# Kernel optimization log

Measured on AMD Instinct MI355X. Metric: run time of the kernel, lower is better.

The kernel has to match this reference:

```python
import jax, jax.numpy as jnp
import numpy as np

D_MODEL = 512
NUM_HEADS = 8
D_HEAD = D_MODEL // NUM_HEADS


def setup_inputs() -> dict:
    key = jax.random.key(0)
    kx, kq, kk, kv, ko = jax.random.split(key, 5)
    s = 1.0 / np.sqrt(D_MODEL)
    return {
        "X": jax.random.normal(kx, (2, 4096, D_MODEL), dtype=jnp.float32),
        "Wq": jax.random.normal(kq, (D_MODEL, D_MODEL), dtype=jnp.float32) * s,
        "Wk": jax.random.normal(kk, (D_MODEL, D_MODEL), dtype=jnp.float32) * s,
        "Wv": jax.random.normal(kv, (D_MODEL, D_MODEL), dtype=jnp.float32) * s,
        "Wo": jax.random.normal(ko, (D_MODEL, D_MODEL), dtype=jnp.float32) * s,
    }


def reference(X, Wq, Wk, Wv, Wo):
    B, L, D = X.shape
    H, dh = NUM_HEADS, D_HEAD
    # Linear projections (torch Linear: y = x @ W.T), split heads -> [B, H, L, dh]
    def proj(W):
        return (X @ W.T).reshape(B, L, H, dh).transpose(0, 2, 1, 3)
    Q, K, V = proj(Wq), proj(Wk), proj(Wv)
    # Scaled dot-product attention; scores [B, H, L, L]
    scores = jnp.einsum("bhqd,bhkd->bhqk", Q, K) / jnp.sqrt(jnp.asarray(dh, X.dtype))
    attn = jax.nn.softmax(scores, axis=-1)
    out = jnp.einsum("bhqk,bhkd->bhqd", attn, V)  # [B, H, L, dh]
    out = out.transpose(0, 2, 1, 3).reshape(B, L, D)
    return out @ Wo.T
```

## Files before the change

### kernel.cpp

```cpp
#include <hip/hip_runtime.h>
#include <math.h>

#define D_MODEL 512
#define NHEADS  8
#define DH      64
#define LSEQ    4096
#define NB      2
#define M_TOT   (NB * LSEQ)
#define NSPLIT  2
#define KHALF   (LSEQ / NSPLIT)

typedef __attribute__((ext_vector_type(8))) short bf16x8;
typedef __attribute__((ext_vector_type(4))) float f32x4;
typedef __attribute__((ext_vector_type(8))) unsigned short ushort8v;

#define MFMA16(a, b, c) __builtin_amdgcn_mfma_f32_16x16x32_bf16(a, b, c, 0, 0, 0)

__device__ __forceinline__ ushort f2bf(float x) {
    unsigned u = __builtin_bit_cast(unsigned, x);
    u += 0x7fffu + ((u >> 16) & 1u);
    return (ushort)(u >> 16);
}

__device__ __forceinline__ float bf2f(ushort u) {
    unsigned v = ((unsigned)u) << 16;
    return __builtin_bit_cast(float, v);
}

__device__ __forceinline__ unsigned cvt_pk_bf16(float a, float b) {
    unsigned r;
    asm("v_cvt_pk_bf16_f32 %0, %1, %2" : "=v"(r) : "v"(a), "v"(b));
    return r;
}

__device__ __forceinline__ float fexp2(float x) {
#if __has_builtin(__builtin_amdgcn_exp2f)
    return __builtin_amdgcn_exp2f(x);
#else
    return exp2f(x);
#endif
}

__device__ __forceinline__ void gload16(const void* g, void* l) {
    __builtin_amdgcn_global_load_lds(
        (const __attribute__((address_space(1))) unsigned*)g,
        (__attribute__((address_space(3))) unsigned*)l, 16, 0, 0);
}

__global__ __launch_bounds__(256) void cast_all(
    const float* __restrict__ X,  const float* __restrict__ Wq,
    const float* __restrict__ Wk, const float* __restrict__ Wv,
    const float* __restrict__ Wo,
    ushort* __restrict__ Xb,  ushort* __restrict__ Wqb,
    ushort* __restrict__ Wkb, ushort* __restrict__ Wvb,
    ushort* __restrict__ Wob)
{
    const int seg = blockIdx.y;
    const float* src = seg == 0 ? X : seg == 1 ? Wq : seg == 2 ? Wk
                      : seg == 3 ? Wv : Wo;
    ushort* dst = seg == 0 ? Xb : seg == 1 ? Wqb : seg == 2 ? Wkb
                 : seg == 3 ? Wvb : Wob;
    const int n = (seg == 0) ? M_TOT * D_MODEL : D_MODEL * D_MODEL;
    const int idx = (blockIdx.x * 256 + threadIdx.x) * 8;
    if (idx >= n) return;
    float4 a = *(const float4*)(src + idx);
    float4 b = *(const float4*)(src + idx + 4);
    ushort8v o;
    o[0] = f2bf(a.x); o[1] = f2bf(a.y); o[2] = f2bf(a.z); o[3] = f2bf(a.w);
    o[4] = f2bf(b.x); o[5] = f2bf(b.y); o[6] = f2bf(b.z); o[7] = f2bf(b.w);
    *(ushort8v*)(dst + idx) = o;
}

__device__ __forceinline__ void gemm_core(
    const ushort* __restrict__ A, const ushort* __restrict__ Bw,
    ushort (*Alds)[64], ushort (*Blds)[64], f32x4 acc[4][4],
    int m0, int n0, int w, int lg, int lr)
{
    const int tid = threadIdx.x;
    const int wr = w >> 1, wc = w & 1;
    const int srow = tid >> 3;
    const int scol = (tid & 7) * 8;

    for (int k0 = 0; k0 < D_MODEL; k0 += 64) {
        __syncthreads();
        #pragma unroll
        for (int i = 0; i < 4; ++i) {
            gload16(A  + (size_t)(m0 + i * 32 + srow) * D_MODEL + k0 + scol,
                    (char*)Alds + i * 4096 + w * 1024);
            gload16(Bw + (size_t)(n0 + i * 32 + srow) * D_MODEL + k0 + scol,
                    (char*)Blds + i * 4096 + w * 1024);
        }
        __syncthreads();
        #pragma unroll
        for (int kk = 0; kk < 2; ++kk) {
            bf16x8 af[4], bfr[4];
            #pragma unroll
            for (int i = 0; i < 4; ++i)
                af[i] = *(const bf16x8*)&Alds[wr * 64 + 16 * i + lr][kk * 32 + 8 * lg];
            #pragma unroll
            for (int j = 0; j < 4; ++j)
                bfr[j] = *(const bf16x8*)&Blds[wc * 64 + 16 * j + lr][kk * 32 + 8 * lg];
            #pragma unroll
            for (int i = 0; i < 4; ++i)
                #pragma unroll
                for (int j = 0; j < 4; ++j)
                    acc[i][j] = MFMA16(af[i], bfr[j], acc[i][j]);
        }
    }
}

__global__ __launch_bounds__(256) void gemm_qkv(
    const ushort* __restrict__ Xb,
    const ushort* __restrict__ Wqb, const ushort* __restrict__ Wkb,
    const ushort* __restrict__ Wvb,
    ushort* __restrict__ Qb, ushort* __restrict__ Kb, ushort* __restrict__ Vtb)
{
    __shared__ __align__(16) ushort Alds[128][64];
    __shared__ __align__(16) ushort Blds[128][64];

    const int mode = blockIdx.z;
    const ushort* Bw = mode == 0 ? Wqb : mode == 1 ? Wkb : Wvb;

    const int tid = threadIdx.x;
    const int w = tid >> 6, l = tid & 63;
    const int lg = l >> 4, lr = l & 15;
    const int wr = w >> 1, wc = w & 1;
    const int m0 = blockIdx.x * 128;
    const int n0 = blockIdx.y * 128;

    f32x4 acc[4][4];
    #pragma unroll
    for (int i = 0; i < 4; ++i)
        #pragma unroll
        for (int j = 0; j < 4; ++j) acc[i][j] = (f32x4){0.f, 0.f, 0.f, 0.f};

    gemm_core(Xb, Bw, Alds, Blds, acc, m0, n0, w, lg, lr);

    if (mode < 2) {
        const float scale = (mode == 0) ? 0.125f * 1.44269504088896f : 1.0f;
        ushort* Yb = (mode == 0) ? Qb : Kb;
        #pragma unroll
        for (int i = 0; i < 4; ++i) {
            const int mb = m0 + wr * 64 + 16 * i + 4 * lg;
            const int b = mb >> 12, lq = mb & 4095;
            #pragma unroll
            for (int j = 0; j < 4; ++j) {
                const int ng = n0 + wc * 64 + 16 * j + lr;
                const int h = ng >> 6, dh = ng & 63;
                ushort* Yp = Yb + ((size_t)(b * NHEADS + h) * LSEQ + lq) * DH + dh;
                #pragma unroll
                for (int r = 0; r < 4; ++r)
                    Yp[(size_t)r * DH] = f2bf(acc[i][j][r] * scale);
            }
        }
    } else {
        #pragma unroll
        for (int i = 0; i < 4; ++i) {
            const int mb = m0 + wr * 64 + 16 * i + 4 * lg;
            const int b = mb >> 12, lq = mb & 4095;
            #pragma unroll
            for (int j = 0; j < 4; ++j) {
                const int ng = n0 + wc * 64 + 16 * j + lr;
                const int h = ng >> 6, dh = ng & 63;
                ushort4 w4;
                w4.x = f2bf(acc[i][j][0]); w4.y = f2bf(acc[i][j][1]);
                w4.z = f2bf(acc[i][j][2]); w4.w = f2bf(acc[i][j][3]);
                *(ushort4*)(Vtb + ((size_t)(b * NHEADS + h) * DH + dh) * LSEQ + lq) = w4;
            }
        }
    }
}

__global__ __launch_bounds__(256) void gemm_wo(
    const ushort* __restrict__ Cb, const ushort* __restrict__ Wob,
    float* __restrict__ out)
{
    __shared__ __align__(16) ushort Alds[128][64];
    __shared__ __align__(16) ushort Blds[128][64];

    const int tid = threadIdx.x;
    const int w = tid >> 6, l = tid & 63;
    const int lg = l >> 4, lr = l & 15;
    const int wr = w >> 1, wc = w & 1;
    const int m0 = blockIdx.x * 128;
    const int n0 = blockIdx.y * 128;

    f32x4 acc[4][4];
    #pragma unroll
    for (int i = 0; i < 4; ++i)
        #pragma unroll
        for (int j = 0; j < 4; ++j) acc[i][j] = (f32x4){0.f, 0.f, 0.f, 0.f};

    gemm_core(Cb, Wob, Alds, Blds, acc, m0, n0, w, lg, lr);

    #pragma unroll
    for (int i = 0; i < 4; ++i) {
        const int mb = m0 + wr * 64 + 16 * i + 4 * lg;
        #pragma unroll
        for (int j = 0; j < 4; ++j) {
            const int ng = n0 + wc * 64 + 16 * j + lr;
            float* Yp = out + (size_t)mb * D_MODEL + ng;
            #pragma unroll
            for (int r = 0; r < 4; ++r)
                Yp[(size_t)r * D_MODEL] = acc[i][j][r];
        }
    }
}

#define QBLK 128
#define KBLK 64

__global__ __launch_bounds__(256) void flash_mfma(
    const ushort* __restrict__ Q, const ushort* __restrict__ K,
    const ushort* __restrict__ Vt, ushort* __restrict__ Op,
    float* __restrict__ Ls)
{
    __shared__ __align__(16) ushort Klds[64][68];
    __shared__ __align__(16) ushort Vlds[64][68];
    __shared__ __align__(16) ushort Plds[128][68];

    const int tid = threadIdx.x;
    const int w  = tid >> 6;
    const int l  = tid & 63;
    const int lg = l >> 4;
    const int lr = l & 15;

    const int bh = blockIdx.y;
    const int q0 = blockIdx.x * QBLK;
    const int z  = blockIdx.z;
    const int kt0  = z * KHALF;
    const int kend = kt0 + KHALF;

    bf16x8 qa[2][2];
    #pragma unroll
    for (int u = 0; u < 2; ++u) {
        const ushort* qp = Q + ((size_t)bh * LSEQ + q0 + 32 * w + 16 * u + lr) * DH + 8 * lg;
        qa[u][0] = *(const bf16x8*)(qp);
        qa[u][1] = *(const bf16x8*)(qp + 32);
    }

    float lsum[2] = {0.f, 0.f};
    f32x4 o4[2][4];
    #pragma unroll
    for (int u = 0; u < 2; ++u)
        #pragma unroll
        for (int ot = 0; ot < 4; ++ot) o4[u][ot] = (f32x4){0.f, 0.f, 0.f, 0.f};

    const int srow = tid >> 2;
    const int scol = (tid & 3) << 4;
    const ushort* Kp = K  + (size_t)bh * LSEQ * DH;
    const ushort* Vp = Vt + (size_t)bh * DH * LSEQ;

    uint4 kA, kB, vA, vB;
    {
        const ushort* ks = Kp + (size_t)(kt0 + srow) * DH + scol;
        const ushort* vs = Vp + (size_t)srow * LSEQ + kt0 + scol;
        kA = *(const uint4*)(ks); kB = *(const uint4*)(ks + 8);
        vA = *(const uint4*)(vs); vB = *(const uint4*)(vs + 8);
    }

    for (int kt = kt0; kt < kend; kt += KBLK) {
        __syncthreads();
        *(uint4*)&Klds[srow][scol] = kA;  *(uint4*)&Klds[srow][scol + 8] = kB;
        *(uint4*)&Vlds[srow][scol] = vA;  *(uint4*)&Vlds[srow][scol + 8] = vB;
        __syncthreads();

        if (kt + KBLK < kend) {
            const ushort* ks = Kp + (size_t)(kt + KBLK + srow) * DH + scol;
            const ushort* vs = Vp + (size_t)srow * LSEQ + (kt + KBLK) + scol;
            kA = *(const uint4*)(ks); kB = *(const uint4*)(ks + 8);
            vA = *(const uint4*)(vs); vB = *(const uint4*)(vs + 8);
        }

        f32x4 s[2][4];
        #pragma unroll
        for (int kt2 = 0; kt2 < 4; ++kt2) {
            bf16x8 k0 = *(const bf16x8*)&Klds[kt2 * 16 + lr][8 * lg];
            bf16x8 k1 = *(const bf16x8*)&Klds[kt2 * 16 + lr][32 + 8 * lg];
            f32x4 z4 = (f32x4){0.f, 0.f, 0.f, 0.f};
            s[0][kt2] = MFMA16(k1, qa[0][1], MFMA16(k0, qa[0][0], z4));
            s[1][kt2] = MFMA16(k1, qa[1][1], MFMA16(k0, qa[1][0], z4));
        }

        #pragma unroll
        for (int u = 0; u < 2; ++u) {
            float rs = 0.f;
            #pragma unroll
            for (int kt2 = 0; kt2 < 4; ++kt2) {
                const float p0 = fexp2(s[u][kt2][0]);
                const float p1 = fexp2(s[u][kt2][1]);
                const float p2 = fexp2(s[u][kt2][2]);
                const float p3 = fexp2(s[u][kt2][3]);
                rs += (p0 + p1) + (p2 + p3);
                uint2 pw;
                pw.x = cvt_pk_bf16(p0, p1);
                pw.y = cvt_pk_bf16(p2, p3);
                *(uint2*)&Plds[32 * w + 16 * u + lr][kt2 * 16 + 4 * lg] = pw;
            }
            lsum[u] += rs;
        }

        #pragma unroll
        for (int vh = 0; vh < 2; ++vh) {
            bf16x8 p0 = *(const bf16x8*)&Plds[32 * w + lr][32 * vh + 8 * lg];
            bf16x8 p1 = *(const bf16x8*)&Plds[32 * w + 16 + lr][32 * vh + 8 * lg];
            #pragma unroll
            for (int ot = 0; ot < 4; ++ot) {
                bf16x8 vv = *(const bf16x8*)&Vlds[16 * ot + lr][32 * vh + 8 * lg];
                o4[0][ot] = MFMA16(p0, vv, o4[0][ot]);
                o4[1][ot] = MFMA16(p1, vv, o4[1][ot]);
            }
        }
    }

    const int b = bh >> 3, h = bh & 7;
    ushort* Opz = Op + (size_t)z * M_TOT * D_MODEL;
    #pragma unroll
    for (int u = 0; u < 2; ++u) {
        float t = lsum[u];
        t += __shfl_xor(t, 16);
        t += __shfl_xor(t, 32);
        if (lg == 0)
            Ls[((size_t)z * NB * NHEADS + bh) * LSEQ + q0 + 32 * w + 16 * u + lr] = t;
        #pragma unroll
        for (int r = 0; r < 4; ++r) {
            const int qrow = q0 + 32 * w + 16 * u + 4 * lg + r;
            ushort* op = Opz + ((size_t)b * LSEQ + qrow) * D_MODEL + h * DH + lr;
            #pragma unroll
            for (int ot = 0; ot < 4; ++ot)
                op[16 * ot] = f2bf(o4[u][ot][r]);
        }
    }
}

__global__ __launch_bounds__(256) void combine(
    const ushort* __restrict__ Op, const float* __restrict__ Ls,
    ushort* __restrict__ Cb)
{
    const int idx = blockIdx.x * 256 + threadIdx.x;
    const int row = idx >> 6;
    const int col0 = (idx & 63) << 3;
    const int b = row >> 12, lq = row & 4095;
    const int h = col0 >> 6;
    const int bh = b * NHEADS + h;

    const float l0 = Ls[(size_t)bh * LSEQ + lq];
    const float l1 = Ls[((size_t)NB * NHEADS + bh) * LSEQ + lq];
    const float inv = 1.0f / (l0 + l1);

    const size_t off = (size_t)row * D_MODEL + col0;
    ushort8v a0 = *(const ushort8v*)(Op + off);
    ushort8v a1 = *(const ushort8v*)(Op + (size_t)M_TOT * D_MODEL + off);
    ushort8v o;
    #pragma unroll
    for (int i = 0; i < 8; ++i)
        o[i] = f2bf((bf2f(a0[i]) + bf2f(a1[i])) * inv);
    *(ushort8v*)(Cb + off) = o;
}

extern "C" void kernel_launch(void* const* d_in, const int* in_sizes, int n_in,
                              void* d_out, int out_size, void* d_ws, size_t ws_size,
                              hipStream_t stream)
{
    const float* X  = (const float*)d_in[0];
    const float* Wq = (const float*)d_in[1];
    const float* Wk = (const float*)d_in[2];
    const float* Wv = (const float*)d_in[3];
    const float* Wo = (const float*)d_in[4];
    float* out = (float*)d_out;

    char* ws = (char*)d_ws;
    const size_t szX = (size_t)M_TOT * D_MODEL * 2;
    const size_t szW = (size_t)D_MODEL * D_MODEL * 2;
    ushort* Xb  = (ushort*)(ws);
    ushort* Wqb = (ushort*)(ws + szX);
    ushort* Wkb = (ushort*)(ws + szX + szW);
    ushort* Wvb = (ushort*)(ws + szX + 2 * szW);
    ushort* Wob = (ushort*)(ws + szX + 3 * szW);
    ushort* Qb  = (ushort*)(ws + szX + 4 * szW);
    ushort* Kb  = (ushort*)(ws + 2 * szX + 4 * szW);
    ushort* Vtb = (ushort*)(ws + 3 * szX + 4 * szW);
    ushort* Opb = (ushort*)(ws + 4 * szX + 4 * szW);
    float*  Lsb = (float*) (ws + 6 * szX + 4 * szW);
    ushort* Cbb = (ushort*)(ws + 6 * szX + 4 * szW + (size_t)NSPLIT * NB * NHEADS * LSEQ * 4);

    dim3 gc(M_TOT * D_MODEL / (256 * 8), 5);
    cast_all<<<gc, 256, 0, stream>>>(X, Wq, Wk, Wv, Wo, Xb, Wqb, Wkb, Wvb, Wob);

    dim3 gq(M_TOT / 128, D_MODEL / 128, 3);
    gemm_qkv<<<gq, 256, 0, stream>>>(Xb, Wqb, Wkb, Wvb, Qb, Kb, Vtb);

    dim3 gf(LSEQ / QBLK, NB * NHEADS, NSPLIT);
    flash_mfma<<<gf, 256, 0, stream>>>(Qb, Kb, Vtb, Opb, Lsb);

    dim3 gm(M_TOT * D_MODEL / (256 * 8));
    combine<<<gm, 256, 0, stream>>>(Opb, Lsb, Cbb);

    dim3 go(M_TOT / 128, D_MODEL / 128);
    gemm_wo<<<go, 256, 0, stream>>>(Cbb, Wob, out);
}
```

Before: 153.8 us.

## Double-buffer K/V tiles in LDS and raise MFMA wave priority

Converts the flash-attention K/V staging into a two-slot LDS ring. The next tile is written into the spare buffer while the current one is consumed, and the global prefetch runs two tiles ahead. This drops one of the two barriers per iteration. It also wraps the MFMA sections in s_setprio to favour matrix-issue waves. The cost is doubled K/V LDS use, which may reduce occupancy, plus more register-held prefetch state.

```diff
diff --git a/kernel.cpp b/kernel.cpp
--- a/kernel.cpp
+++ b/kernel.cpp
@@ -209,14 +209,15 @@
 
 #define QBLK 128
 #define KBLK 64
+#define NT   (KHALF / KBLK)
 
 __global__ __launch_bounds__(256) void flash_mfma(
     const ushort* __restrict__ Q, const ushort* __restrict__ K,
     const ushort* __restrict__ Vt, ushort* __restrict__ Op,
     float* __restrict__ Ls)
 {
-    __shared__ __align__(16) ushort Klds[64][68];
-    __shared__ __align__(16) ushort Vlds[64][68];
+    __shared__ __align__(16) ushort Klds[2][64][68];
+    __shared__ __align__(16) ushort Vlds[2][64][68];
     __shared__ __align__(16) ushort Plds[128][68];
 
     const int tid = threadIdx.x;
@@ -228,8 +229,7 @@
     const int bh = blockIdx.y;
     const int q0 = blockIdx.x * QBLK;
     const int z  = blockIdx.z;
-    const int kt0  = z * KHALF;
-    const int kend = kt0 + KHALF;
+    const int kt0 = z * KHALF;
 
     bf16x8 qa[2][2];
     #pragma unroll
@@ -257,30 +257,43 @@
         const ushort* vs = Vp + (size_t)srow * LSEQ + kt0 + scol;
         kA = *(const uint4*)(ks); kB = *(const uint4*)(ks + 8);
         vA = *(const uint4*)(vs); vB = *(const uint4*)(vs + 8);
-    }
-
-    for (int kt = kt0; kt < kend; kt += KBLK) {
-        __syncthreads();
-        *(uint4*)&Klds[srow][scol] = kA;  *(uint4*)&Klds[srow][scol + 8] = kB;
-        *(uint4*)&Vlds[srow][scol] = vA;  *(uint4*)&Vlds[srow][scol + 8] = vB;
-        __syncthreads();
-
-        if (kt + KBLK < kend) {
-            const ushort* ks = Kp + (size_t)(kt + KBLK + srow) * DH + scol;
-            const ushort* vs = Vp + (size_t)srow * LSEQ + (kt + KBLK) + scol;
+        *(uint4*)&Klds[0][srow][scol] = kA;  *(uint4*)&Klds[0][srow][scol + 8] = kB;
+        *(uint4*)&Vlds[0][srow][scol] = vA;  *(uint4*)&Vlds[0][srow][scol + 8] = vB;
+        const ushort* ks1 = Kp + (size_t)(kt0 + KBLK + srow) * DH + scol;
+        const ushort* vs1 = Vp + (size_t)srow * LSEQ + (kt0 + KBLK) + scol;
+        kA = *(const uint4*)(ks1); kB = *(const uint4*)(ks1 + 8);
+        vA = *(const uint4*)(vs1); vB = *(const uint4*)(vs1 + 8);
+    }
+    __syncthreads();
+
+    for (int t = 0; t < NT; ++t) {
+        const int cur = t & 1;
+
+        if (t + 1 < NT) {
+            *(uint4*)&Klds[cur ^ 1][srow][scol]     = kA;
+            *(uint4*)&Klds[cur ^ 1][srow][scol + 8] = kB;
+            *(uint4*)&Vlds[cur ^ 1][srow][scol]     = vA;
+            *(uint4*)&Vlds[cur ^ 1][srow][scol + 8] = vB;
+        }
+        if (t + 2 < NT) {
+            const int kt2g = kt0 + (t + 2) * KBLK;
+            const ushort* ks = Kp + (size_t)(kt2g + srow) * DH + scol;
+            const ushort* vs = Vp + (size_t)srow * LSEQ + kt2g + scol;
             kA = *(const uint4*)(ks); kB = *(const uint4*)(ks + 8);
             vA = *(const uint4*)(vs); vB = *(const uint4*)(vs + 8);
         }
 
         f32x4 s[2][4];
+        __builtin_amdgcn_s_setprio(1);
         #pragma unroll
         for (int kt2 = 0; kt2 < 4; ++kt2) {
-            bf16x8 k0 = *(const bf16x8*)&Klds[kt2 * 16 + lr][8 * lg];
-            bf16x8 k1 = *(const bf16x8*)&Klds[kt2 * 16 + lr][32 + 8 * lg];
+            bf16x8 k0 = *(const bf16x8*)&Klds[cur][kt2 * 16 + lr][8 * lg];
+            bf16x8 k1 = *(const bf16x8*)&Klds[cur][kt2 * 16 + lr][32 + 8 * lg];
             f32x4 z4 = (f32x4){0.f, 0.f, 0.f, 0.f};
             s[0][kt2] = MFMA16(k1, qa[0][1], MFMA16(k0, qa[0][0], z4));
             s[1][kt2] = MFMA16(k1, qa[1][1], MFMA16(k0, qa[1][0], z4));
         }
+        __builtin_amdgcn_s_setprio(0);
 
         #pragma unroll
         for (int u = 0; u < 2; ++u) {
@@ -300,17 +313,21 @@
             lsum[u] += rs;
         }
 
+        __builtin_amdgcn_s_setprio(1);
         #pragma unroll
         for (int vh = 0; vh < 2; ++vh) {
             bf16x8 p0 = *(const bf16x8*)&Plds[32 * w + lr][32 * vh + 8 * lg];
             bf16x8 p1 = *(const bf16x8*)&Plds[32 * w + 16 + lr][32 * vh + 8 * lg];
             #pragma unroll
             for (int ot = 0; ot < 4; ++ot) {
-                bf16x8 vv = *(const bf16x8*)&Vlds[16 * ot + lr][32 * vh + 8 * lg];
+                bf16x8 vv = *(const bf16x8*)&Vlds[cur][16 * ot + lr][32 * vh + 8 * lg];
                 o4[0][ot] = MFMA16(p0, vv, o4[0][ot]);
                 o4[1][ot] = MFMA16(p1, vv, o4[1][ot]);
             }
         }
+        __builtin_amdgcn_s_setprio(0);
+
+        __syncthreads();
     }
 
     const int b = bh >> 3, h = bh & 7;
```

New measurement: 155.9 us. About the same (+1.3%).
